# Optimization experiments

Hardware: AMD Instinct MI355X
Metric: run time of the kernel (lower is better)

Reference implementation:

```python
import jax, jax.numpy as jnp
import numpy as np

B, S, D = 1, 2048, 2048
H, KV, HD = 32, 8, 64
POWER = 100000.0


def _rotary(x):
    # x: [B, h, S, HD]; faithful to RotaryEncoder: freqs = pos / div_term
    rot_dim = HD // 2
    pos = jnp.arange(S, dtype=x.dtype)
    div = POWER ** (jnp.arange(0, HD, 2, dtype=x.dtype) / HD)  # [HD//2]
    freqs = pos[:, None] / div  # [S, HD//2]
    cos, sin = jnp.cos(freqs), jnp.sin(freqs)
    x_rot, x_pass = x[..., :rot_dim], x[..., rot_dim:]
    h = rot_dim // 2
    rot_half = jnp.concatenate([-x_rot[..., h:], x_rot[..., :h]], axis=-1)
    return jnp.concatenate([x_rot * cos + rot_half * sin, x_pass], axis=-1)


def setup_inputs() -> dict:
    key = jax.random.key(0)
    k1, k2, k3 = jax.random.split(key, 3)
    hidden_states = jax.random.normal(k1, (B, S, D), dtype=jnp.float32)
    op_size = H * HD + 2 * KV * HD
    Wqkv = jax.random.normal(k2, (D, op_size), dtype=jnp.float32) * 0.02
    Wo = jax.random.normal(k3, (H * HD, D), dtype=jnp.float32) * 0.02
    causal = jnp.tril(jnp.ones((S, S), dtype=bool))
    attention_mask = jnp.where(causal, 0.0, -1e9).astype(jnp.float32)[None, None]
    return {"hidden_states": hidden_states, "attention_mask": attention_mask,
            "Wqkv": Wqkv, "Wo": Wo}


def reference(hidden_states, attention_mask, Wqkv, Wo):
    groups = H // KV
    qkv = hidden_states @ Wqkv  # [B, S, op_size]
    qpos = H * HD
    q = qkv[..., :qpos].reshape(B, S, H, HD).transpose(0, 2, 1, 3)
    k = qkv[..., qpos:qpos + KV * HD].reshape(B, S, KV, HD).transpose(0, 2, 1, 3)
    v = qkv[..., qpos + KV * HD:].reshape(B, S, KV, HD).transpose(0, 2, 1, 3)
    q = _rotary(q)
    k = _rotary(k)
    k = jnp.repeat(k, groups, axis=1)  # GQA repeat_interleave -> [B, H, S, HD]
    v = jnp.repeat(v, groups, axis=1)
    scores = jnp.einsum('bhqd,bhkd->bhqk', q, k) / jnp.sqrt(jnp.float32(HD))
    scores = scores + attention_mask[..., :S]
    attn = jax.nn.softmax(scores.astype(jnp.float32), axis=-1).astype(v.dtype)
    out = jnp.einsum('bhqk,bhkd->bhqd', attn, v)
    out = out.transpose(0, 2, 1, 3).reshape(B, S, H * HD)
    return out @ Wo
```

## Files before the change

kernel.cpp:

```cpp
#include <hip/hip_runtime.h>
#include <hip/hip_bf16.h>
#include <cstdint>
#include <cstddef>

#define S_LEN 2048
#define D_MODEL 2048
#define NH 32
#define NKV 8
#define HDIM 64
#define OPSZ 3072
#define KOFF 2048
#define VOFF 2560

typedef float    floatx4  __attribute__((ext_vector_type(4)));
typedef float    floatx16 __attribute__((ext_vector_type(16)));
typedef __bf16   bf16x8  __attribute__((ext_vector_type(8)));
typedef __bf16   bf16x4  __attribute__((ext_vector_type(4)));
typedef __bf16   bf16_t;
typedef _Float16 f16_t;
typedef _Float16 f16x2   __attribute__((ext_vector_type(2)));
typedef _Float16 f16x4   __attribute__((ext_vector_type(4)));
typedef _Float16 f16x8   __attribute__((ext_vector_type(8)));
typedef __fp16   hfx2    __attribute__((ext_vector_type(2)));

__device__ __forceinline__ void gld16(const void* g, void* l) {
  __builtin_amdgcn_global_load_lds((__attribute__((address_space(1))) void*)(void*)g,
                                   (__attribute__((address_space(3))) void*)l,
                                   16, 0, 0);
}

#define ACQ(N) do { asm volatile("s_waitcnt vmcnt(" #N ")" ::: "memory");        \
                    __builtin_amdgcn_s_barrier();                                \
                    __builtin_amdgcn_sched_barrier(0); } while (0)
#define REL()  do { __builtin_amdgcn_sched_barrier(0);                           \
                    __builtin_amdgcn_s_barrier();                                \
                    __builtin_amdgcn_sched_barrier(0); } while (0)

__global__ __launch_bounds__(256)
void prep_kernel(const float* __restrict__ X, const float* __restrict__ Wqkv,
                 const float* __restrict__ Wo, bf16_t* __restrict__ Xb,
                 bf16_t* __restrict__ WqkvT, bf16_t* __restrict__ WoT) {
  const int bx = blockIdx.x;
  const int k0 = blockIdx.y * 32;
  const int tid = threadIdx.x;
  const int r  = tid >> 3;
  const int c4 = (tid & 7) * 4;
  if (bx < 160) {
    __shared__ float tile[32][33];
    const float* W; bf16_t* Wt; int N, n0;
    if (bx < 96) { W = Wqkv; Wt = WqkvT; N = OPSZ;    n0 = bx * 32; }
    else         { W = Wo;   Wt = WoT;   N = D_MODEL; n0 = (bx - 96) * 32; }
    const float4 v = *(const float4*)&W[(size_t)(k0 + r) * N + n0 + c4];
    tile[r][c4 + 0] = v.x; tile[r][c4 + 1] = v.y;
    tile[r][c4 + 2] = v.z; tile[r][c4 + 3] = v.w;
    __syncthreads();
    bf16x4 o;
#pragma unroll
    for (int j = 0; j < 4; j++) o[j] = (bf16_t)tile[c4 + j][r];
    *(bf16x4*)&Wt[(size_t)(n0 + r) * D_MODEL + k0 + c4] = o;
  } else {
    const int n0 = (bx - 160) * 32;
    const size_t idx = (size_t)(k0 + r) * D_MODEL + n0 + c4;
    const float4 v = *(const float4*)&X[idx];
    bf16x4 o;
    o[0] = (bf16_t)v.x; o[1] = (bf16_t)v.y; o[2] = (bf16_t)v.z; o[3] = (bf16_t)v.w;
    *(bf16x4*)&Xb[idx] = o;
  }
}

#define GEMM128_CORE(A_, Bt_, K_, m0_, n0_)                                       \
  const int tid = threadIdx.x;                                                    \
  const int wave = tid >> 6;                                                      \
  const int lane = tid & 63;                                                      \
  const int lane15 = lane & 15;                                                   \
  const int quad = lane >> 4;                                                     \
  const int wm = (wave & 1) * 64;                                                 \
  const int wn = (wave >> 1) * 64;                                                \
  floatx4 acc[4][4];                                                              \
  _Pragma("unroll") for (int i = 0; i < 4; i++)                                   \
    _Pragma("unroll") for (int j = 0; j < 4; j++)                                 \
      acc[i][j] = floatx4{0.f, 0.f, 0.f, 0.f};                                    \
  {                                                                               \
    int srow[4], scol[4];                                                         \
    _Pragma("unroll") for (int i = 0; i < 4; i++) {                               \
      const int c = tid + i * 256;                                                \
      srow[i] = c >> 3;                                                           \
      scol[i] = (((c & 7) * 16) ^ ((srow[i] & 7) << 4)) >> 1;                     \
    }                                                                             \
    const bf16_t* Ab = (A_) + (size_t)(m0_) * (K_);                               \
    const bf16_t* Bb = (Bt_) + (size_t)(n0_) * (K_);                              \
    const int rsw = (lane15 & 7) << 4;                                            \
    auto stage = [&](bf16_t* dA, bf16_t* dB, int k0) {                            \
      _Pragma("unroll") for (int i = 0; i < 4; i++)                               \
        gld16(Ab + (size_t)srow[i] * (K_) + k0 + scol[i],                         \
              dA + (i * 256 + wave * 64) * 8);                                    \
      _Pragma("unroll") for (int i = 0; i < 4; i++)                               \
        gld16(Bb + (size_t)srow[i] * (K_) + k0 + scol[i],                         \
              dB + (i * 256 + wave * 64) * 8);                                    \
    };                                                                            \
    auto comp = [&](const bf16_t* sA, const bf16_t* sB) {                         \
      _Pragma("unroll") for (int kt = 0; kt < 2; kt++) {                          \
        const int off = ((kt * 64 + quad * 16) ^ rsw) >> 1;                       \
        bf16x8 af[4], bfr[4];                                                     \
        _Pragma("unroll") for (int mi = 0; mi < 4; mi++)                          \
          af[mi] = *(const bf16x8*)&sA[(wm + mi * 16 + lane15) * 64 + off];       \
        _Pragma("unroll") for (int ni = 0; ni < 4; ni++)                          \
          bfr[ni] = *(const bf16x8*)&sB[(wn + ni * 16 + lane15) * 64 + off];      \
        _Pragma("unroll") for (int mi = 0; mi < 4; mi++)                          \
          _Pragma("unroll") for (int ni = 0; ni < 4; ni++)                        \
            acc[mi][ni] = __builtin_amdgcn_mfma_f32_16x16x32_bf16(af[mi], bfr[ni],\
                                                                  acc[mi][ni], 0, 0, 0); \
      }                                                                           \
    };                                                                            \
    const int NT = (K_) / 64;                                                     \
    stage(As0, Bs0, 0);                                                           \
    stage(As1, Bs1, 64);                                                          \
    for (int t = 0; t < NT - 2; t += 2) {                                         \
      ACQ(8);                                                                     \
      comp(As0, Bs0);                                                             \
      REL();                                                                      \
      stage(As0, Bs0, (t + 2) * 64);                                              \
      ACQ(8);                                                                     \
      comp(As1, Bs1);                                                             \
      REL();                                                                      \
      stage(As1, Bs1, (t + 3) * 64);                                              \
    }                                                                             \
    ACQ(8);                                                                       \
    comp(As0, Bs0);                                                               \
    ACQ(0);                                                                       \
    comp(As1, Bs1);                                                               \
  }

#define GEMM128_LDS                                                               \
  __shared__ bf16_t As0[128 * 64];                                                \
  __shared__ bf16_t As1[128 * 64];                                                \
  __shared__ bf16_t Bs0[128 * 64];                                                \
  __shared__ bf16_t Bs1[128 * 64];

#define XCD_SWZ(m0_, n0_)                                                         \
  const int gx_ = gridDim.x;                                                      \
  const int id_ = blockIdx.y * gx_ + blockIdx.x;                                  \
  const int cpx_ = (gx_ * gridDim.y) >> 3;                                        \
  const int sid_ = (id_ & 7) * cpx_ + (id_ >> 3);                                 \
  const int m0_ = (sid_ / gx_) * 128;                                             \
  const int n0_ = (sid_ % gx_) * 128;

#define QSCALE 0.18033688011112042f
__global__ __launch_bounds__(256, 2)
void gemm_qkv_rope(const bf16_t* __restrict__ A, const bf16_t* __restrict__ Bt,
                   bf16_t* __restrict__ Qr, bf16_t* __restrict__ Kr,
                   f16_t* __restrict__ VtG) {
  GEMM128_LDS
  XCD_SWZ(m0, n0)
  GEMM128_CORE(A, Bt, D_MODEL, m0, n0)

  const int colbase = n0 + wn;
  const int s0 = m0 + wm;

  if (colbase < VOFF) {
    const bool isQ = (colbase < KOFF);
    const float k2 = 0.51905126483f;
    const float pj0 = exp2f(-(float)lane15 * k2);
    const float pj1 = pj0 * 0.0031622776601684f;
    bf16_t* dst = isQ ? (Qr + ((size_t)(colbase >> 6) * S_LEN) * HDIM)
                      : (Kr + ((size_t)((colbase - KOFF) >> 6) * S_LEN) * HDIM);
    const float qs = isQ ? QSCALE : 1.0f;
#pragma unroll
    for (int mi = 0; mi < 4; mi++) {
#pragma unroll
      for (int r = 0; r < 4; r++) {
        const int s = s0 + mi * 16 + quad * 4 + r;
        const float sf = (float)s;
        float s0s, s0c, s1s, s1c;
        __sincosf(sf * pj0, &s0s, &s0c);
        __sincosf(sf * pj1, &s1s, &s1c);
        const float x0 = acc[mi][0][r], x1 = acc[mi][1][r];
        bf16_t* row = dst + (size_t)s * HDIM + lane15;
        row[0]  = (bf16_t)((x0 * s0c - x1 * s0s) * qs);
        row[16] = (bf16_t)((x1 * s1c + x0 * s1s) * qs);
        row[32] = (bf16_t)(acc[mi][2][r] * qs);
        row[48] = (bf16_t)(acc[mi][3][r] * qs);
      }
    }
  } else {
    const int kvv = (colbase - VOFF) >> 6;
    f16_t* dst = VtG + (size_t)kvv * HDIM * S_LEN;
#pragma unroll
    for (int mi = 0; mi < 4; mi++) {
      const int s = s0 + mi * 16 + quad * 4;
#pragma unroll
      for (int ni = 0; ni < 4; ni++) {
        const int d = ni * 16 + lane15;
        f16x4 tv;
#pragma unroll
        for (int r = 0; r < 4; r++) tv[r] = (f16_t)acc[mi][ni][r];
        *(f16x4*)&dst[(size_t)d * S_LEN + s] = tv;
      }
    }
  }
}

__global__ __launch_bounds__(256, 2)
void gemm_bt_f32out(const bf16_t* __restrict__ A, const bf16_t* __restrict__ Bt,
                    float* __restrict__ C, int M, int N, int K) {
  GEMM128_LDS
  XCD_SWZ(m0, n0)
  GEMM128_CORE(A, Bt, K, m0, n0)

#pragma unroll
  for (int mi = 0; mi < 4; mi++)
#pragma unroll
    for (int r = 0; r < 4; r++) {
      const int row = m0 + wm + mi * 16 + quad * 4 + r;
#pragma unroll
      for (int ni = 0; ni < 4; ni++) {
        const int col = n0 + wn + ni * 16 + lane15;
        C[(size_t)row * N + col] = acc[mi][ni][r];
      }
    }
}

__global__ __launch_bounds__(256, 2)
void flash_kernel(const bf16_t* __restrict__ Qr, const bf16_t* __restrict__ Kr,
                  const f16_t* __restrict__ VtG, bf16_t* __restrict__ attn) {
  __shared__ bf16_t Ks[128 * 64];
  __shared__ f16_t  Vt[64 * 128];

  const int tid = threadIdx.x;
  const int wave = tid >> 6;
  const int lane = tid & 63;
  const int l31 = lane & 31;
  const int half = lane >> 5;
  const int bx = blockIdx.x;
  const int h = bx & 31;
  const int bq = bx >> 5;
  const int qblk = (bq < 8) ? (15 - bq) : (bq - 8);
  const int q0 = qblk * 128;
  const int rq = q0 + wave * 32;
  const int kv = h >> 2;
  const size_t kbase = (size_t)kv * S_LEN * HDIM;
  const size_t vbase = (size_t)kv * HDIM * S_LEN;

  const int krow0 = tid >> 3;
  const int kcol  = ((((tid & 7) * 16) ^ (((tid >> 3) & 7) << 4)) >> 1);
  const int vd0   = tid >> 4;
  const int vcol  = ((((tid & 15) * 16) ^ ((vd0 & 15) << 4)) >> 1);

  const int kswz = (l31 & 7) << 4;
  const int vswz = (l31 & 15) << 4;

  bf16x8 aq[4];
#pragma unroll
  for (int kt = 0; kt < 4; kt++)
    aq[kt] = *(const bf16x8*)&Qr[((size_t)h * S_LEN + rq + l31) * HDIM + kt * 16 + half * 8];

  floatx16 o0, o1;
#pragma unroll
  for (int i = 0; i < 16; i++) { o0[i] = 0.f; o1[i] = 0.f; }
  floatx4 ls = floatx4{0.f, 0.f, 0.f, 0.f};

  const int nk = qblk + 1;

  for (int t = 0; t < nk; ++t) {
    const int p0 = t * 128;
    __syncthreads();
#pragma unroll
    for (int i = 0; i < 4; i++)
      gld16(Kr + kbase + (size_t)(p0 + krow0 + i * 32) * HDIM + kcol,
            &Ks[(i * 256 + wave * 64) * 8]);
#pragma unroll
    for (int i = 0; i < 4; i++)
      gld16(VtG + vbase + (size_t)(vd0 + i * 16) * S_LEN + p0 + vcol,
            &Vt[(i * 256 + wave * 64) * 8]);
    __syncthreads();

#pragma unroll
    for (int nt = 0; nt < 4; nt++) {
      floatx16 sc;
#pragma unroll
      for (int i = 0; i < 16; i++) sc[i] = 0.f;
#pragma unroll
      for (int kt = 0; kt < 4; kt++) {
        const bf16x8 ak = *(const bf16x8*)&Ks[(nt * 32 + l31) * 64 +
                                              (((kt * 32 + half * 16) ^ kswz) >> 1)];
        sc = __builtin_amdgcn_mfma_f32_32x32x16_bf16(ak, aq[kt], sc, 0, 0, 0);
      }

      if (p0 + nt * 32 + 31 > rq) {
        const int qrow = rq + l31;
        const int kb = p0 + nt * 32 + 4 * half;
#pragma unroll
        for (int r = 0; r < 16; r++) {
          const int kpos = kb + (r & 3) + 8 * (r >> 2);
          if (kpos > qrow) sc[r] = -1e30f;
        }
      }

      f16x4 ph[4];
#pragma unroll
      for (int g = 0; g < 4; g++) {
        const float e0 = __builtin_amdgcn_exp2f(sc[4 * g + 0]);
        const float e1 = __builtin_amdgcn_exp2f(sc[4 * g + 1]);
        const float e2 = __builtin_amdgcn_exp2f(sc[4 * g + 2]);
        const float e3 = __builtin_amdgcn_exp2f(sc[4 * g + 3]);
        ls[g] += (e0 + e1) + (e2 + e3);
        const hfx2 lo_ = __builtin_amdgcn_cvt_pkrtz(e0, e1);
        const hfx2 hi_ = __builtin_amdgcn_cvt_pkrtz(e2, e3);
        ph[g] = __builtin_shufflevector(__builtin_bit_cast(f16x2, lo_),
                                        __builtin_bit_cast(f16x2, hi_), 0, 1, 2, 3);
      }

#pragma unroll
      for (int g = 0; g < 4; g++) {
        const int cb = nt * 64 + g * 16 + half * 8;
        const f16x4 av0 = *(const f16x4*)&Vt[(l31) * 128 + ((cb ^ vswz) >> 1)];
        const f16x4 av1 = *(const f16x4*)&Vt[(32 + l31) * 128 + ((cb ^ vswz) >> 1)];
        o0 = __builtin_amdgcn_mfma_f32_32x32x8f16(av0, ph[g], o0, 0, 0, 0);
        o1 = __builtin_amdgcn_mfma_f32_32x32x8f16(av1, ph[g], o1, 0, 0, 0);
      }
    }
  }

  float lsum = ls[0] + ls[1] + ls[2] + ls[3];
  lsum += __shfl_xor(lsum, 32);
  const float inv = 1.0f / lsum;
  const int s = rq + l31;
#pragma unroll
  for (int rg = 0; rg < 4; rg++) {
    bf16x4 t0, t1;
#pragma unroll
    for (int j = 0; j < 4; j++) {
      t0[j] = (bf16_t)(o0[rg * 4 + j] * inv);
      t1[j] = (bf16_t)(o1[rg * 4 + j] * inv);
    }
    const int d = rg * 8 + half * 4;
    *(bf16x4*)&attn[(size_t)s * D_MODEL + h * HDIM + d] = t0;
    *(bf16x4*)&attn[(size_t)s * D_MODEL + h * HDIM + 32 + d] = t1;
  }
}

extern "C" void kernel_launch(void* const* d_in, const int* in_sizes, int n_in,
                              void* d_out, int out_size, void* d_ws, size_t ws_size,
                              hipStream_t stream) {
  (void)in_sizes; (void)n_in; (void)out_size; (void)ws_size;
  const float* hidden = (const float*)d_in[0];
  const float* Wqkv = (const float*)d_in[2];
  const float* Wo   = (const float*)d_in[3];
  float* out = (float*)d_out;

  char* ws = (char*)d_ws;
  size_t off = 0;
  auto alloc = [&](size_t bytes) -> void* {
    void* p = ws + off;
    off += (bytes + 255) & ~(size_t)255;
    return p;
  };
  bf16_t* Xb    = (bf16_t*)alloc((size_t)S_LEN * D_MODEL * 2);
  bf16_t* WqkvT = (bf16_t*)alloc((size_t)OPSZ * D_MODEL * 2);
  bf16_t* WoT   = (bf16_t*)alloc((size_t)D_MODEL * D_MODEL * 2);
  bf16_t* Qr    = (bf16_t*)alloc((size_t)NH * S_LEN * HDIM * 2);
  bf16_t* Kr    = (bf16_t*)alloc((size_t)NKV * S_LEN * HDIM * 2);
  f16_t*  VtG   = (f16_t*) alloc((size_t)NKV * HDIM * S_LEN * 2);
  bf16_t* attn  = (bf16_t*)alloc((size_t)S_LEN * D_MODEL * 2);

  prep_kernel<<<dim3(224, 64), 256, 0, stream>>>(hidden, Wqkv, Wo, Xb, WqkvT, WoT);
  gemm_qkv_rope<<<dim3(OPSZ / 128, S_LEN / 128), 256, 0, stream>>>(Xb, WqkvT, Qr, Kr, VtG);
  flash_kernel<<<dim3(16 * NH), 256, 0, stream>>>(Qr, Kr, VtG, attn);
  gemm_bt_f32out<<<dim3(D_MODEL / 128, S_LEN / 128), 256, 0, stream>>>(attn, WoT, out, S_LEN, D_MODEL, D_MODEL);
}
```

Before: 202.8 us.

## Switch GEMM LDS pipeline from double to triple buffering with rotating pointers

Turns the GEMM main loop from a two-stage into a three-stage LDS ring by adding a third A/B buffer pair and rotating buffer pointers each iteration. The wait counts are adjusted so two tiles stay in flight while one is computed, aiming to hide more global-load latency. This uses 96KB of LDS per block, so launch bounds drop to one block per SIMD group, which lowers occupancy and may cancel the latency-hiding benefit.

```diff
diff --git a/kernel.cpp b/kernel.cpp
--- a/kernel.cpp
+++ b/kernel.cpp
@@ -113,29 +113,29 @@
       }                                                                           \
     };                                                                            \
     const int NT = (K_) / 64;                                                     \
-    stage(As0, Bs0, 0);                                                           \
-    stage(As1, Bs1, 64);                                                          \
-    for (int t = 0; t < NT - 2; t += 2) {                                         \
-      ACQ(8);                                                                     \
-      comp(As0, Bs0);                                                             \
-      REL();                                                                      \
-      stage(As0, Bs0, (t + 2) * 64);                                              \
-      ACQ(8);                                                                     \
-      comp(As1, Bs1);                                                             \
-      REL();                                                                      \
-      stage(As1, Bs1, (t + 3) * 64);                                              \
+    bf16_t *a0 = As0, *a1 = As1, *a2 = As2;                                       \
+    bf16_t *b0 = Bs0, *b1 = Bs1, *b2 = Bs2;                                       \
+    stage(a0, b0, 0);                                                             \
+    stage(a1, b1, 64);                                                            \
+    stage(a2, b2, 128);                                                           \
+    for (int t = 0; t < NT; ++t) {                                                \
+      if (t + 2 < NT)      ACQ(16);                  \
+      else if (t + 1 < NT) ACQ(8);                                                \
+      else                 ACQ(0);                                                \
+      comp(a0, b0);                                                               \
+      if (t + 3 < NT) { REL(); stage(a0, b0, (t + 3) * 64); }                     \
+      bf16_t* ta = a0; a0 = a1; a1 = a2; a2 = ta;                                 \
+      bf16_t* tb = b0; b0 = b1; b1 = b2; b2 = tb;                                 \
     }                                                                             \
-    ACQ(8);                                                                       \
-    comp(As0, Bs0);                                                               \
-    ACQ(0);                                                                       \
-    comp(As1, Bs1);                                                               \
   }
 
 #define GEMM128_LDS                                                               \
   __shared__ bf16_t As0[128 * 64];                                                \
   __shared__ bf16_t As1[128 * 64];                                                \
+  __shared__ bf16_t As2[128 * 64];                                                \
   __shared__ bf16_t Bs0[128 * 64];                                                \
-  __shared__ bf16_t Bs1[128 * 64];
+  __shared__ bf16_t Bs1[128 * 64];                                                \
+  __shared__ bf16_t Bs2[128 * 64];
 
 #define XCD_SWZ(m0_, n0_)                                                         \
   const int gx_ = gridDim.x;                                                      \
@@ -146,7 +146,7 @@
   const int n0_ = (sid_ % gx_) * 128;
 
 #define QSCALE 0.18033688011112042f
-__global__ __launch_bounds__(256, 2)
+__global__ __launch_bounds__(256, 1)
 void gemm_qkv_rope(const bf16_t* __restrict__ A, const bf16_t* __restrict__ Bt,
                    bf16_t* __restrict__ Qr, bf16_t* __restrict__ Kr,
                    f16_t* __restrict__ VtG) {
@@ -200,7 +200,7 @@
   }
 }
 
-__global__ __launch_bounds__(256, 2)
+__global__ __launch_bounds__(256, 1)
 void gemm_bt_f32out(const bf16_t* __restrict__ A, const bf16_t* __restrict__ Bt,
                     float* __restrict__ C, int M, int N, int K) {
   GEMM128_LDS
```

New measurement: 249.9 us. 23.2% more time.
